# Optimization experiments

Measured on AMD Instinct MI355X. Metric: run time of the kernel, lower is better.

The kernel has to match this reference:

```python
import jax, jax.numpy as jnp
import numpy as np

N = 50000        # nodes
E = 1600000      # edges
IN = 256         # in_features
AD = 128         # attention_dim
H = 8            # heads
DK = AD // H     # per-head dim


def setup_inputs() -> dict:
    key = jax.random.key(0)
    ks = jax.random.split(key, 9)
    hi = jax.random.normal(ks[0], (N, IN), jnp.float32)
    radial = jax.random.uniform(ks[1], (E, 1), jnp.float32)
    edge = jax.random.randint(ks[2], (2, E), 0, N)
    # learned params (torch Linear: y = x @ W.T + b)
    Qw = jax.random.normal(ks[3], (AD, IN), jnp.float32) * 0.05
    Qb = jax.random.normal(ks[4], (AD,), jnp.float32) * 0.05
    Qrw = jax.random.normal(ks[5], (AD, 1), jnp.float32) * 0.05
    Qrb = jax.random.normal(ks[6], (AD,), jnp.float32) * 0.05
    Kw = jax.random.normal(ks[7], (AD, IN), jnp.float32) * 0.05
    Kb = jax.random.normal(ks[8], (AD,), jnp.float32) * 0.05
    return {"hi": hi, "radial": radial, "Qw": Qw, "Qb": Qb,
            "Qrw": Qrw, "Qrb": Qrb, "Kw": Kw, "Kb": Kb, "edge": edge}


def _segment_softmax(logits, seg, num_segments):
    # numerically stable softmax grouped by segment id (per head column)
    m = jax.ops.segment_max(logits, seg, num_segments=num_segments)  # [N, H]
    ex = jnp.exp(logits - m[seg])
    s = jax.ops.segment_sum(ex, seg, num_segments=num_segments)      # [N, H]
    return ex / s[seg]


def reference(hi, radial, Qw, Qb, Qrw, Qrb, Kw, Kb, edge):
    # node projections: [N, AD] -> [N, H, DK]
    q = (hi @ Qw.T + Qb).reshape(-1, H, DK)
    k = (hi @ Kw.T + Kb).reshape(-1, H, DK)
    # per-edge radial projection: [E, AD] -> [E, H, DK]
    q_rad = (radial @ Qrw.T + Qrb).reshape(-1, H, DK)
    # gather by edge endpoints; original transposes (1,2) then sums dim=1,
    # which is exactly a contraction over DK per head.
    src = q[edge[0]] + q_rad          # [E, H, DK]
    dst_k = k[edge[1]]                # [E, H, DK]
    prods = jnp.sum(src * dst_k, axis=-1) / np.sqrt(DK)  # [E, H]
    # square_plus=False, reweight_attention=False, attention_norm_idx=0
    attention = _segment_softmax(prods, edge[0], N)
    return attention, prods
```

## Files before the change

### kernel.cpp

```cpp
#include <hip/hip_runtime.h>
#include <hip/hip_fp16.h>
#include <math.h>

#define N_NODES 50000
#define EDGES   1600000
#define IN_F    256
#define AD      128
#define H       8
#define DK      16

typedef __attribute__((ext_vector_type(8))) _Float16 half8;
typedef __attribute__((ext_vector_type(4))) _Float16 half4;
typedef __attribute__((ext_vector_type(4))) float floatx4;

__global__ void zero_kernel(float* __restrict__ p, int n) {
    int i = blockIdx.x * blockDim.x + threadIdx.x;
    if (i < n) p[i] = 0.0f;
}

__global__ void wswz_kernel(const float* __restrict__ Qw,
                            const float* __restrict__ Kw,
                            half8* __restrict__ Wfrag) {
    const int idx = blockIdx.x * blockDim.x + threadIdx.x;
    if (idx >= 8 * 16 * 64) return;
    const int lane = idx & 63;
    const int nb   = (idx >> 6) & 15;
    const int kb   = idx >> 10;
    const int n    = nb * 16 + (lane & 15);
    const int k0   = kb * 32 + ((lane >> 4) << 3);
    const float* row = (n < AD) ? (Qw + (size_t)n * IN_F)
                                : (Kw + (size_t)(n - AD) * IN_F);
    half8 v;
#pragma unroll
    for (int j = 0; j < 8; j++) v[j] = (_Float16)row[k0 + j];
    Wfrag[idx] = v;
}

#define APAD 264
__global__ __launch_bounds__(256) void proj_mfma_kernel(
    const float* __restrict__ hi, const half8* __restrict__ Wfrag,
    const float* __restrict__ Qb, const float* __restrict__ Kb,
    __half* __restrict__ qh, __half* __restrict__ kh)
{
    __shared__ _Float16 Atile[64][APAD];
    const int r0 = blockIdx.x * 64;
    const int t  = threadIdx.x;

    {
        const int row = t >> 2;
        const int c4  = t & 3;
        const bool valid = (r0 + row) < N_NODES;
        const float4* src = (const float4*)(hi + (size_t)(r0 + row) * IN_F);
#pragma unroll
        for (int i = 0; i < 16; i++) {
            const int col4 = c4 + i * 4;
            float4 v = valid ? src[col4] : make_float4(0.f, 0.f, 0.f, 0.f);
            half4 hv;
            hv[0] = (_Float16)v.x; hv[1] = (_Float16)v.y;
            hv[2] = (_Float16)v.z; hv[3] = (_Float16)v.w;
            *(half4*)&Atile[row][col4 * 4] = hv;
        }
    }
    __syncthreads();

    const int wave = t >> 6;
    const int lane = t & 63;
    const int m    = lane & 15;
    const int quad = lane >> 4;

    floatx4 acc[4][4];
#pragma unroll
    for (int a = 0; a < 4; a++)
#pragma unroll
        for (int b = 0; b < 4; b++) acc[a][b] = (floatx4)0.f;

#pragma unroll
    for (int kb = 0; kb < 8; kb++) {
        half8 Af[4], Bf[4];
#pragma unroll
        for (int rb = 0; rb < 4; rb++)
            Af[rb] = *(const half8*)&Atile[rb * 16 + m][kb * 32 + quad * 8];
#pragma unroll
        for (int nbi = 0; nbi < 4; nbi++)
            Bf[nbi] = Wfrag[(size_t)(kb * 16 + wave * 4 + nbi) * 64 + lane];
#pragma unroll
        for (int rb = 0; rb < 4; rb++)
#pragma unroll
            for (int nbi = 0; nbi < 4; nbi++)
                acc[rb][nbi] = __builtin_amdgcn_mfma_f32_16x16x32_f16(
                    Af[rb], Bf[nbi], acc[rb][nbi], 0, 0, 0);
    }

#pragma unroll
    for (int nbi = 0; nbi < 4; nbi++) {
        const int n   = wave * 64 + nbi * 16 + m;
        const float bias = (n < AD) ? Qb[n] : Kb[n - AD];
        __half* out   = (n < AD) ? qh : kh;
        const int ncol = n & (AD - 1);
#pragma unroll
        for (int rb = 0; rb < 4; rb++) {
#pragma unroll
            for (int reg = 0; reg < 4; reg++) {
                const int row = r0 + rb * 16 + quad * 4 + reg;
                if (row < N_NODES)
                    out[(size_t)row * AD + ncol] = __float2half(acc[rb][nbi][reg] + bias);
            }
        }
    }
}

__global__ __launch_bounds__(256) void edge_kernel(
    const __half* __restrict__ qh, const __half* __restrict__ kh,
    const float* __restrict__ radial, const int* __restrict__ edge,
    const float* __restrict__ Qrw, const float* __restrict__ Qrb,
    float* __restrict__ att, float* __restrict__ prods, float* __restrict__ ssum)
{
    const int t = blockIdx.x * blockDim.x + threadIdx.x;
    const int e = t >> 3;
    const int h = t & 7;
    if (e >= EDGES) return;

    const int e0 = edge[e];
    const int e1 = edge[EDGES + e];

    const half8* qp = (const half8*)(qh + (size_t)e0 * AD + h * DK);
    const half8* kp = (const half8*)(kh + (size_t)e1 * AD + h * DK);
    half8 q0 = qp[0], q1 = qp[1];
    half8 k0 = kp[0], k1 = kp[1];

    const float4* rw4 = (const float4*)(Qrw + h * DK);
    const float4* rb4 = (const float4*)(Qrb + h * DK);
    float rw[16], rb[16];
#pragma unroll
    for (int j = 0; j < 4; j++) {
        float4 w = rw4[j];
        rw[4 * j + 0] = w.x; rw[4 * j + 1] = w.y; rw[4 * j + 2] = w.z; rw[4 * j + 3] = w.w;
        float4 b = rb4[j];
        rb[4 * j + 0] = b.x; rb[4 * j + 1] = b.y; rb[4 * j + 2] = b.z; rb[4 * j + 3] = b.w;
    }

    float a = 0.f, b = 0.f, c = 0.f;
#pragma unroll
    for (int i = 0; i < 8; i++) {
        float qf = (float)q0[i], kf = (float)k0[i];
        a += qf * kf;
        b += rw[i] * kf;
        c += rb[i] * kf;
    }
#pragma unroll
    for (int i = 0; i < 8; i++) {
        float qf = (float)q1[i], kf = (float)k1[i];
        a += qf * kf;
        b += rw[8 + i] * kf;
        c += rb[8 + i] * kf;
    }

    const float r = radial[e];
    const float p = (a + r * b + c) * 0.25f;
    prods[t] = p;
    const float ex = __expf(p);
    att[t] = ex;
    atomicAdd(&ssum[e0 * H + h], ex);
}

__global__ __launch_bounds__(256) void norm_kernel(
    float* __restrict__ att, const float* __restrict__ ssum,
    const int* __restrict__ edge)
{
    const int i = blockIdx.x * blockDim.x + threadIdx.x;
    if (i < EDGES * H) {
        const int e  = i >> 3;
        const int h  = i & 7;
        const int e0 = edge[e];
        att[i] = att[i] / ssum[e0 * H + h];
    }
}

extern "C" void kernel_launch(void* const* d_in, const int* in_sizes, int n_in,
                              void* d_out, int out_size, void* d_ws, size_t ws_size,
                              hipStream_t stream) {
    const float* hi     = (const float*)d_in[0];
    const float* radial = (const float*)d_in[1];
    const float* Qw     = (const float*)d_in[2];
    const float* Qb     = (const float*)d_in[3];
    const float* Qrw    = (const float*)d_in[4];
    const float* Qrb    = (const float*)d_in[5];
    const float* Kw     = (const float*)d_in[6];
    const float* Kb     = (const float*)d_in[7];
    const int*   edge   = (const int*)d_in[8];

    float* att   = (float*)d_out;
    float* prods = att + (size_t)EDGES * H;

    __half* qh   = (__half*)d_ws;
    __half* kh   = qh + (size_t)N_NODES * AD;
    float*  ssum = (float*)(kh + (size_t)N_NODES * AD);
    half8*  Wfrag = (half8*)(ssum + (size_t)N_NODES * H);

    zero_kernel<<<(N_NODES * H + 255) / 256, 256, 0, stream>>>(ssum, N_NODES * H);
    wswz_kernel<<<(8 * 16 * 64 + 255) / 256, 256, 0, stream>>>(Qw, Kw, Wfrag);
    proj_mfma_kernel<<<(N_NODES + 63) / 64, 256, 0, stream>>>(hi, Wfrag, Qb, Kb, qh, kh);
    edge_kernel<<<(EDGES * H + 255) / 256, 256, 0, stream>>>(qh, kh, radial, edge,
                                                             Qrw, Qrb, att, prods, ssum);
    norm_kernel<<<(EDGES * H + 255) / 256, 256, 0, stream>>>(att, ssum, edge);
}
```

Before: 361.5 us.

## Precompute per-node radial terms, process two edges per thread, recompute exp in norm

Adds a per-node prep kernel that folds the radial weight/bias dot products with k into two floats per node and head, and zeroes the segment sums there, which removes the separate zero kernel. The edge kernel now handles two edges per thread, uses packed fp16 dot instructions, and no longer writes the exponentials to the attention buffer. The norm kernel recomputes exp from prods and writes eight heads per thread with vector nontemporal stores. This cuts per-edge arithmetic and one full E*H write/read pass, at the cost of recomputing exp and an extra small launch.

Result: no change. 356.8 us (median of 2 runs) (-1.3%).

```diff
diff --git a/kernel.cpp b/kernel.cpp
--- a/kernel.cpp
+++ b/kernel.cpp
@@ -13,10 +13,9 @@
 typedef __attribute__((ext_vector_type(4))) _Float16 half4;
 typedef __attribute__((ext_vector_type(4))) float floatx4;
 
-__global__ void zero_kernel(float* __restrict__ p, int n) {
-    int i = blockIdx.x * blockDim.x + threadIdx.x;
-    if (i < n) p[i] = 0.0f;
-}
+#ifndef __has_builtin
+#define __has_builtin(x) 0
+#endif
 
 __global__ void wswz_kernel(const float* __restrict__ Qw,
                             const float* __restrict__ Kw,
@@ -109,71 +108,126 @@
     }
 }
 
-__global__ __launch_bounds__(256) void edge_kernel(
+__global__ __launch_bounds__(256) void kprep_kernel(
+    const __half* __restrict__ kh, const float* __restrict__ Qrw,
+    const float* __restrict__ Qrb, float2* __restrict__ cb,
+    float* __restrict__ ssum)
+{
+    const int t = blockIdx.x * blockDim.x + threadIdx.x;
+    if (t >= N_NODES * H) return;
+    ssum[t] = 0.0f;
+    const int h = t & 7;
+    const half8* kp = (const half8*)(kh + (size_t)(t >> 3) * AD + h * DK);
+    half8 k0 = kp[0], k1 = kp[1];
+    const float* rw = Qrw + h * DK;
+    const float* rb = Qrb + h * DK;
+    float brw = 0.f, crb = 0.f;
+#pragma unroll
+    for (int i = 0; i < 8; i++) {
+        float kf = (float)k0[i];
+        brw = fmaf(rw[i], kf, brw);
+        crb = fmaf(rb[i], kf, crb);
+    }
+#pragma unroll
+    for (int i = 0; i < 8; i++) {
+        float kf = (float)k1[i];
+        brw = fmaf(rw[8 + i], kf, brw);
+        crb = fmaf(rb[8 + i], kf, crb);
+    }
+    cb[t] = make_float2(crb * 0.25f, brw * 0.25f);
+}
+
+__device__ __forceinline__ float dot16(half8 x0, half8 y0, half8 x1, half8 y1) {
+#if __has_builtin(__builtin_amdgcn_fdot2)
+    typedef _Float16 half2v __attribute__((ext_vector_type(2)));
+    float acc = 0.f;
+#pragma unroll
+    for (int i = 0; i < 4; i++) {
+        half2v a = {x0[2 * i], x0[2 * i + 1]};
+        half2v b = {y0[2 * i], y0[2 * i + 1]};
+        acc = __builtin_amdgcn_fdot2(a, b, acc, false);
+    }
+#pragma unroll
+    for (int i = 0; i < 4; i++) {
+        half2v a = {x1[2 * i], x1[2 * i + 1]};
+        half2v b = {y1[2 * i], y1[2 * i + 1]};
+        acc = __builtin_amdgcn_fdot2(a, b, acc, false);
+    }
+    return acc;
+#else
+    float acc = 0.f;
+#pragma unroll
+    for (int i = 0; i < 8; i++) acc += (float)x0[i] * (float)y0[i];
+#pragma unroll
+    for (int i = 0; i < 8; i++) acc += (float)x1[i] * (float)y1[i];
+    return acc;
+#endif
+}
+
+__global__ __launch_bounds__(256, 6) void edge_kernel(
     const __half* __restrict__ qh, const __half* __restrict__ kh,
     const float* __restrict__ radial, const int* __restrict__ edge,
-    const float* __restrict__ Qrw, const float* __restrict__ Qrb,
-    float* __restrict__ att, float* __restrict__ prods, float* __restrict__ ssum)
+    const float2* __restrict__ cb,
+    float* __restrict__ prods, float* __restrict__ ssum)
 {
     const int t = blockIdx.x * blockDim.x + threadIdx.x;
     const int e = t >> 3;
     const int h = t & 7;
+    if (e >= EDGES / 2) return;
+    const int eB = e + EDGES / 2;
+
+    const int e0a = edge[e];
+    const int e1a = edge[EDGES + e];
+    const int e0b = edge[eB];
+    const int e1b = edge[EDGES + eB];
+
+    const half8* qpa = (const half8*)(qh + (size_t)e0a * AD + h * DK);
+    const half8* kpa = (const half8*)(kh + (size_t)e1a * AD + h * DK);
+    const half8* qpb = (const half8*)(qh + (size_t)e0b * AD + h * DK);
+    const half8* kpb = (const half8*)(kh + (size_t)e1b * AD + h * DK);
+    half8 qa0 = qpa[0], qa1 = qpa[1];
+    half8 ka0 = kpa[0], ka1 = kpa[1];
+    half8 qb0 = qpb[0], qb1 = qpb[1];
+    half8 kb0 = kpb[0], kb1 = kpb[1];
+    const float2 cba = cb[(size_t)e1a * H + h];
+    const float2 cbb = cb[(size_t)e1b * H + h];
+    const float ra = __builtin_nontemporal_load(&radial[e]);
+    const float rb = __builtin_nontemporal_load(&radial[eB]);
+
+    const float aa = dot16(qa0, ka0, qa1, ka1);
+    const float ab = dot16(qb0, kb0, qb1, kb1);
+
+    const float pa = fmaf(0.25f, aa, fmaf(ra, cba.y, cba.x));
+    const float pb = fmaf(0.25f, ab, fmaf(rb, cbb.y, cbb.x));
+
+    __builtin_nontemporal_store(pa, &prods[(size_t)e * H + h]);
+    __builtin_nontemporal_store(pb, &prods[(size_t)eB * H + h]);
+
+    atomicAdd(&ssum[e0a * H + h], __expf(pa));
+    atomicAdd(&ssum[e0b * H + h], __expf(pb));
+}
+
+__global__ __launch_bounds__(256) void norm_kernel(
+    const float* __restrict__ prods, const float* __restrict__ ssum,
+    const int* __restrict__ edge, float* __restrict__ att)
+{
+    const int e = blockIdx.x * blockDim.x + threadIdx.x;
     if (e >= EDGES) return;
-
     const int e0 = edge[e];
-    const int e1 = edge[EDGES + e];
-
-    const half8* qp = (const half8*)(qh + (size_t)e0 * AD + h * DK);
-    const half8* kp = (const half8*)(kh + (size_t)e1 * AD + h * DK);
-    half8 q0 = qp[0], q1 = qp[1];
-    half8 k0 = kp[0], k1 = kp[1];
-
-    const float4* rw4 = (const float4*)(Qrw + h * DK);
-    const float4* rb4 = (const float4*)(Qrb + h * DK);
-    float rw[16], rb[16];
-#pragma unroll
-    for (int j = 0; j < 4; j++) {
-        float4 w = rw4[j];
-        rw[4 * j + 0] = w.x; rw[4 * j + 1] = w.y; rw[4 * j + 2] = w.z; rw[4 * j + 3] = w.w;
-        float4 b = rb4[j];
-        rb[4 * j + 0] = b.x; rb[4 * j + 1] = b.y; rb[4 * j + 2] = b.z; rb[4 * j + 3] = b.w;
-    }
-
-    float a = 0.f, b = 0.f, c = 0.f;
-#pragma unroll
-    for (int i = 0; i < 8; i++) {
-        float qf = (float)q0[i], kf = (float)k0[i];
-        a += qf * kf;
-        b += rw[i] * kf;
-        c += rb[i] * kf;
-    }
-#pragma unroll
-    for (int i = 0; i < 8; i++) {
-        float qf = (float)q1[i], kf = (float)k1[i];
-        a += qf * kf;
-        b += rw[8 + i] * kf;
-        c += rb[8 + i] * kf;
-    }
-
-    const float r = radial[e];
-    const float p = (a + r * b + c) * 0.25f;
-    prods[t] = p;
-    const float ex = __expf(p);
-    att[t] = ex;
-    atomicAdd(&ssum[e0 * H + h], ex);
-}
-
-__global__ __launch_bounds__(256) void norm_kernel(
-    float* __restrict__ att, const float* __restrict__ ssum,
-    const int* __restrict__ edge)
-{
-    const int i = blockIdx.x * blockDim.x + threadIdx.x;
-    if (i < EDGES * H) {
-        const int e  = i >> 3;
-        const int h  = i & 7;
-        const int e0 = edge[e];
-        att[i] = att[i] / ssum[e0 * H + h];
-    }
+    const floatx4* pp = (const floatx4*)(prods + (size_t)e * H);
+    floatx4 p0 = __builtin_nontemporal_load(pp);
+    floatx4 p1 = __builtin_nontemporal_load(pp + 1);
+    const floatx4* sp = (const floatx4*)(ssum + (size_t)e0 * H);
+    floatx4 s0 = sp[0], s1 = sp[1];
+    floatx4 a0, a1;
+#pragma unroll
+    for (int i = 0; i < 4; i++) {
+        a0[i] = __expf(p0[i]) / s0[i];
+        a1[i] = __expf(p1[i]) / s1[i];
+    }
+    floatx4* ap = (floatx4*)(att + (size_t)e * H);
+    __builtin_nontemporal_store(a0, ap);
+    __builtin_nontemporal_store(a1, ap + 1);
 }
 
 extern "C" void kernel_launch(void* const* d_in, const int* in_sizes, int n_in,
@@ -196,11 +250,12 @@
     __half* kh   = qh + (size_t)N_NODES * AD;
     float*  ssum = (float*)(kh + (size_t)N_NODES * AD);
     half8*  Wfrag = (half8*)(ssum + (size_t)N_NODES * H);
-
-    zero_kernel<<<(N_NODES * H + 255) / 256, 256, 0, stream>>>(ssum, N_NODES * H);
+    float2* cbuf = (float2*)(Wfrag + 8 * 16 * 64);
+
     wswz_kernel<<<(8 * 16 * 64 + 255) / 256, 256, 0, stream>>>(Qw, Kw, Wfrag);
     proj_mfma_kernel<<<(N_NODES + 63) / 64, 256, 0, stream>>>(hi, Wfrag, Qb, Kb, qh, kh);
-    edge_kernel<<<(EDGES * H + 255) / 256, 256, 0, stream>>>(qh, kh, radial, edge,
-                                                             Qrw, Qrb, att, prods, ssum);
-    norm_kernel<<<(EDGES * H + 255) / 256, 256, 0, stream>>>(att, ssum, edge);
-}
+    kprep_kernel<<<(N_NODES * H + 255) / 256, 256, 0, stream>>>(kh, Qrw, Qrb, cbuf, ssum);
+    edge_kernel<<<(EDGES * H / 2 + 255) / 256, 256, 0, stream>>>(qh, kh, radial, edge,
+                                                                 cbuf, prods, ssum);
+    norm_kernel<<<(EDGES + 255) / 256, 256, 0, stream>>>(prods, ssum, edge, att);
+}
```
